# Kernel optimization log

Measured on AMD Instinct MI355X. Metric: run time of the kernel, lower is better.

## Reference

```python
import jax, jax.numpy as jnp
import numpy as np

EPS = 1e-14
RHO = 8.0


def _normalize(x):
    return x / jnp.linalg.norm(x, axis=-1, keepdims=True)


def setup_inputs() -> dict:
    key = jax.random.key(0)
    ks = jax.random.split(key, 12)
    B, D = 4096, 1024
    f = lambda k: _normalize(jax.random.normal(k, (B, D), dtype=jnp.float32))
    pos = lambda k: jax.random.uniform(k, (B, 1), dtype=jnp.float32, minval=0.1, maxval=1.0)
    return {
        "im_feat": f(ks[0]),
        "tt_feat": f(ks[1]),
        "rim_feat": f(ks[2]),
        "rtt_feat": f(ks[3]),
        "remote_u_im": pos(ks[4]),
        "remote_u_tt": pos(ks[5]),
        "loss1_im": pos(ks[6]),
        "loss1_tt": pos(ks[7]),
        "u_im": pos(ks[8]),
        "u_tt": pos(ks[9]),
        "logit_scale": 10.0 * jnp.ones((1,), dtype=jnp.float32),
        "offset": 0,
    }


def _pairwise_loss(rim, rtt, im, tt, logit_scale, offset):
    # features1 = remote, features2 = local (as in forward(): pairwise_loss(remote_features, features, ...))
    sim_image = rim @ tt.T                                  # [B1, B2]
    sim_text = rtt @ im.T                                   # [B1, B2]
    diag_sim = jnp.sum(rim * rtt, axis=-1, keepdims=True)   # [B1, 1]
    exp_im = jnp.exp((sim_image - diag_sim) * logit_scale)
    exp_tt = jnp.exp((sim_text - diag_sim) * logit_scale)
    B1, B2 = sim_image.shape
    # mask zeros the shifted diagonal: equivalent to subtracting the diagonal entry from the row sum
    cols = (jnp.arange(B1) + offset)[:, None]               # [B1, 1]
    rw_sum = B2 - 1 if B1 <= B2 else B2 * (B1 - 1) / B1
    loss_im = (jnp.sum(exp_im, axis=-1, keepdims=True)
               - jnp.take_along_axis(exp_im, cols, axis=1)) / rw_sum
    loss_tt = (jnp.sum(exp_tt, axis=-1, keepdims=True)
               - jnp.take_along_axis(exp_tt, cols, axis=1)) / rw_sum
    return loss_im, loss_tt


def reference(im_feat, tt_feat, rim_feat, rtt_feat, remote_u_im, remote_u_tt,
              loss1_im, loss1_tt, u_im, u_tt, logit_scale, offset):
    loss2_im, loss2_tt = _pairwise_loss(rim_feat, rtt_feat, im_feat, tt_feat, logit_scale, offset)
    pg1 = loss1_im / (u_im + EPS) + loss1_tt / (u_tt + EPS)
    pg2 = loss2_im / (remote_u_im + EPS) + loss2_tt / (remote_u_tt + EPS)
    loss = (jnp.mean(pg1) + jnp.mean(pg2)) / 2
    # multiply_tau branch
    ls = logit_scale[0]
    loss = loss / jax.lax.stop_gradient(ls)
    loss = loss + RHO / ls
    loss = loss + jnp.mean(jnp.log(u_im) + jnp.log(u_tt)) / 2 / ls
    return loss
```

## Files before the change

kernel.cpp:

```cpp
#include <hip/hip_runtime.h>
#include <hip/hip_bf16.h>

#define EPSF 1e-14f
#define RHOF 8.0f

typedef __attribute__((ext_vector_type(4))) float f32x4;
typedef __attribute__((ext_vector_type(8))) int   i32x8;
typedef __attribute__((ext_vector_type(2))) unsigned long long u64x2;

#define AS_GLOBAL __attribute__((address_space(1)))
#define AS_LDS    __attribute__((address_space(3)))


__global__ __launch_bounds__(256) void prep_fp8(
    const float* __restrict__ im,  const float* __restrict__ tt,
    const float* __restrict__ rim, const float* __restrict__ rtt,
    unsigned char* __restrict__ bIm,  unsigned char* __restrict__ bTt,
    unsigned char* __restrict__ bRim, unsigned char* __restrict__ bRtt,
    float* __restrict__ S_im, float* __restrict__ S_tt,
    float* __restrict__ diag, float* __restrict__ red,
    int D, int spm )
{
    __shared__ unsigned char L[8 * 1024];
    const int b = blockIdx.x;
    const int tid = threadIdx.x;
    const int nConv = 4 * spm;
    if (b < nConv) {
        int mIdx = b / spm;
        int slab = b - mIdx * spm;
        const float* src = (mIdx == 0) ? rim : (mIdx == 1) ? tt
                          : (mIdx == 2) ? rtt : im;
        unsigned char* dst = (mIdx == 0) ? bRim : (mIdx == 1) ? bTt
                            : (mIdx == 2) ? bRtt : bIm;
        const float* srow = src + (size_t)slab * 8 * D;
        const int n4 = (8 * D) >> 2;
        for (int idx = tid; idx < n4; idx += 256) {
            float4 v = *(const float4*)(srow + idx * 4);
            int pk = __builtin_amdgcn_cvt_pk_fp8_f32(v.x, v.y, 0, false);
            pk     = __builtin_amdgcn_cvt_pk_fp8_f32(v.z, v.w, pk, true);
            *(int*)&L[idx * 4] = pk;
        }
        __syncthreads();
        const int kTiles = D >> 7;
        const int rb = (slab * 8) >> 7;
        const int r0loc = (slab * 8) & 127;
        for (int g = tid; g < (D >> 1); g += 256) {
            int kb  = g >> 6;
            int rem = g & 63;
            int rl  = rem >> 3;
            int p   = rem & 7;
            int r   = slab * 8 + rl;
            int c   = p ^ (r & 7);
            const unsigned char* lb = &L[rl * D + kb * 128 + c * 16];
            u64x2 o = *(const u64x2*)lb;
            char* outp = (char*)dst
                       + ((size_t)(rb * kTiles + kb) * 1024
                          + (size_t)(r0loc + rl) * 8 + p) * 16;
            *(u64x2*)outp = o;
        }
    } else {
        int db = b - nConv;
        if (db == 0 && tid < 8) red[tid] = 0.f;
        if (tid < 4) { S_im[db * 4 + tid] = 0.f; S_tt[db * 4 + tid] = 0.f; }
        int row  = db * 4 + (tid >> 6);
        int lane = tid & 63;
        const float* a = rim + (size_t)row * D;
        const float* c = rtt + (size_t)row * D;
        float s = 0.f;
        for (int k = lane * 4; k < D; k += 256) {
            float4 av = *(const float4*)(a + k);
            float4 cv = *(const float4*)(c + k);
            s += av.x * cv.x + av.y * cv.y + av.z * cv.z + av.w * cv.w;
        }
        #pragma unroll
        for (int m2 = 1; m2 < 64; m2 <<= 1) s += __shfl_xor(s, m2, 64);
        if (lane == 0) diag[row] = s;
    }
}

__global__ __launch_bounds__(256) void gemm_expsum(
    const unsigned char* __restrict__ A0, const unsigned char* __restrict__ B0,
    float* __restrict__ S0,
    const unsigned char* __restrict__ A1, const unsigned char* __restrict__ B1,
    float* __restrict__ S1,
    const float* __restrict__ logit_scale, const int* __restrict__ offset,
    int Bn, int D)
{
    const int z = blockIdx.z;
    const unsigned char* A = z ? A1 : A0;
    const unsigned char* B = z ? B1 : B0;
    float* S = z ? S1 : S0;

    __shared__ unsigned char As[2][16384];
    __shared__ unsigned char Bs[2][16384];

    const int tid  = threadIdx.x;
    const int wave = tid >> 6;
    const int lane = tid & 63;
    const int lo   = lane & 15;
    const int qd   = lane >> 4;
    const int m0   = (wave >> 1) * 64;
    const int n0   = (wave & 1) * 64;
    const int s0   = (2 * qd) ^ (lo & 7);
    const int offA = s0 * 16;
    const int offB = (s0 ^ 1) * 16;

    const int kTiles = D >> 7;
    const unsigned char* Atile = A + (size_t)blockIdx.y * kTiles * 16384;
    const unsigned char* Btile = B + (size_t)blockIdx.x * kTiles * 16384;

    auto stage = [&](int buf, const unsigned char* At, const unsigned char* Bt) {
        #pragma unroll
        for (int j = 0; j < 4; ++j) {
            int goff = (j * 256 + tid) * 16;
            int loff = j * 4096 + wave * 1024;
            __builtin_amdgcn_global_load_lds(
                (const AS_GLOBAL unsigned int*)(At + goff),
                (AS_LDS unsigned int*)&As[buf][loff], 16, 0, 0);
            __builtin_amdgcn_global_load_lds(
                (const AS_GLOBAL unsigned int*)(Bt + goff),
                (AS_LDS unsigned int*)&Bs[buf][loff], 16, 0, 0);
        }
    };

    f32x4 acc[4][4];
    #pragma unroll
    for (int i = 0; i < 4; ++i)
        #pragma unroll
        for (int j = 0; j < 4; ++j)
            acc[i][j] = (f32x4){0.f, 0.f, 0.f, 0.f};

    stage(0, Atile, Btile);
    __syncthreads();

    for (int kb = 0; kb < kTiles; ++kb) {
        const int cur = kb & 1;
        if (kb + 1 < kTiles)
            stage(1 - cur, Atile + 16384, Btile + 16384);

        i32x8 bq[4];
        #pragma unroll
        for (int t = 0; t < 4; ++t) {
            int rn = (n0 + 16 * t + lo) * 128;
            union { int4 h[2]; i32x8 v; } u;
            u.h[0] = *(const int4*)&Bs[cur][rn + offA];
            u.h[1] = *(const int4*)&Bs[cur][rn + offB];
            bq[t] = u.v;
        }
        #pragma unroll
        for (int ti = 0; ti < 4; ++ti) {
            int ra = (m0 + 16 * ti + lo) * 128;
            union { int4 h[2]; i32x8 v; } u;
            u.h[0] = *(const int4*)&As[cur][ra + offA];
            u.h[1] = *(const int4*)&As[cur][ra + offB];
            i32x8 af = u.v;
            #pragma unroll
            for (int tj = 0; tj < 4; ++tj)
                acc[ti][tj] = __builtin_amdgcn_mfma_scale_f32_16x16x128_f8f6f4(
                    af, bq[tj], acc[ti][tj],
                    0, 0,
                    0, 127,
                    0, 127);
        }
        __syncthreads();

        Atile += 16384;
        Btile += 16384;
    }

    const float ls = logit_scale[0];
    const int offs = offset[0];
    const int rowBase = blockIdx.y * 128;
    const int colBase = blockIdx.x * 128;
    #pragma unroll
    for (int ti = 0; ti < 4; ++ti) {
        #pragma unroll
        for (int r = 0; r < 4; ++r) {
            int gi = rowBase + m0 + 16 * ti + 4 * qd + r;
            float rs = 0.f;
            #pragma unroll
            for (int tj = 0; tj < 4; ++tj) {
                int gj = colBase + n0 + 16 * tj + lo;
                float e = __expf(ls * acc[ti][tj][r]);
                if (gj == gi + offs) e = 0.f;
                rs += e;
            }
            #pragma unroll
            for (int m = 1; m < 16; m <<= 1) rs += __shfl_xor(rs, m, 64);
            if (lo == 0) atomicAdd(&S[gi], rs);
        }
    }
}

__global__ __launch_bounds__(256) void final_kernel(
    const float* __restrict__ S_im, const float* __restrict__ S_tt,
    const float* __restrict__ diag,
    const float* __restrict__ ru_im, const float* __restrict__ ru_tt,
    const float* __restrict__ l1_im, const float* __restrict__ l1_tt,
    const float* __restrict__ u_im,  const float* __restrict__ u_tt,
    const float* __restrict__ logit_scale, float* __restrict__ red,
    float* __restrict__ out, int Bn)
{
    const float ls = logit_scale[0];
    const float inv_rw = 1.0f / (float)(Bn - 1);
    const int gid = blockIdx.x * 256 + threadIdx.x;
    float pg = 0.f, lg = 0.f;
    for (int i = gid; i < Bn; i += 8 * 256) {
        float p1 = l1_im[i] / (u_im[i] + EPSF) + l1_tt[i] / (u_tt[i] + EPSF);
        float dd = expf(-ls * diag[i]);
        float p2 = dd * S_im[i] * inv_rw / (ru_im[i] + EPSF)
                 + dd * S_tt[i] * inv_rw / (ru_tt[i] + EPSF);
        pg += p1 + p2;
        lg += logf(u_im[i]) + logf(u_tt[i]);
    }
    __shared__ float sp[256], sl[256];
    sp[threadIdx.x] = pg; sl[threadIdx.x] = lg;
    __syncthreads();
    for (int s = 128; s > 0; s >>= 1) {
        if (threadIdx.x < s) { sp[threadIdx.x] += sp[threadIdx.x + s];
                               sl[threadIdx.x] += sl[threadIdx.x + s]; }
        __syncthreads();
    }
    if (threadIdx.x == 0) {
        atomicAdd(&red[0], sp[0]);
        atomicAdd(&red[1], sl[0]);
        __threadfence();
        int t = atomicAdd((int*)&red[2], 1);
        if (t == gridDim.x - 1) {
            float pgSum = atomicAdd(&red[0], 0.f);
            float lgSum = atomicAdd(&red[1], 0.f);
            float loss = ((pgSum / (float)Bn) * 0.5f) / ls
                       + RHOF / ls
                       + (lgSum / (float)Bn) * 0.5f / ls;
            out[0] = loss;
        }
    }
}

extern "C" void kernel_launch(void* const* d_in, const int* in_sizes, int n_in,
                              void* d_out, int out_size, void* d_ws, size_t ws_size,
                              hipStream_t stream) {
    const float* im    = (const float*)d_in[0];
    const float* tt    = (const float*)d_in[1];
    const float* rim   = (const float*)d_in[2];
    const float* rtt   = (const float*)d_in[3];
    const float* ru_im = (const float*)d_in[4];
    const float* ru_tt = (const float*)d_in[5];
    const float* l1_im = (const float*)d_in[6];
    const float* l1_tt = (const float*)d_in[7];
    const float* u_im  = (const float*)d_in[8];
    const float* u_tt  = (const float*)d_in[9];
    const float* lsc   = (const float*)d_in[10];
    const int*   offs  = (const int*)d_in[11];

    const int Bn = in_sizes[4];
    const int D  = in_sizes[0] / Bn;
    const int spm = Bn / 8;

    char* base = (char*)d_ws;
    float* S_im = (float*)base;
    float* S_tt = S_im + Bn;
    float* diag = S_tt + Bn;
    float* red  = diag + Bn;
    const size_t headBytes = (((size_t)(3 * Bn + 8) * sizeof(float)) + 255) & ~(size_t)255;
    const size_t matBytes  = (size_t)Bn * D;
    unsigned char* buf0 = (unsigned char*)(base + headBytes);
    unsigned char* bRim = buf0;
    unsigned char* bTt  = buf0 + matBytes;
    unsigned char* bRtt = buf0 + 2 * matBytes;
    unsigned char* bIm  = buf0 + 3 * matBytes;

    prep_fp8<<<4 * spm + Bn / 4, 256, 0, stream>>>(
        im, tt, rim, rtt, bIm, bTt, bRim, bRtt, S_im, S_tt, diag, red, D, spm);

    dim3 ggrid(Bn / 128, Bn / 128, 2);
    gemm_expsum<<<ggrid, 256, 0, stream>>>(bRim, bTt, S_im, bRtt, bIm, S_tt,
                                           lsc, offs, Bn, D);

    final_kernel<<<8, 256, 0, stream>>>(S_im, S_tt, diag, ru_im, ru_tt,
                                        l1_im, l1_tt, u_im, u_tt, lsc,
                                        red, (float*)d_out, Bn);
}
```

Baseline: 184.4 us.

## Enlarge GEMM tile to 256x256 with 8 waves, grid swizzle and MFMA priority

The fused fp8 GEMM+exp-sum kernel moves from 128x128 tiles with 4 waves to 256x256 tiles with 8 waves. Each wave now computes a 128x64 sub-tile, which raises operand reuse from LDS and cuts global traffic per output. The change also adds an XCD-style workgroup swizzle for L2 locality and wraps the MFMA loop in s_setprio. In exchange, LDS use rises to 128KB per block, accumulator registers double, and the grid shrinks to 512 blocks, so occupancy and tail effects may suffer.

```diff
diff --git a/kernel.cpp b/kernel.cpp
--- a/kernel.cpp
+++ b/kernel.cpp
@@ -78,7 +78,7 @@
     }
 }
 
-__global__ __launch_bounds__(256) void gemm_expsum(
+__global__ __launch_bounds__(512, 2) void gemm_expsum(
     const unsigned char* __restrict__ A0, const unsigned char* __restrict__ B0,
     float* __restrict__ S0,
     const unsigned char* __restrict__ A1, const unsigned char* __restrict__ B1,
@@ -91,69 +91,81 @@
     const unsigned char* B = z ? B1 : B0;
     float* S = z ? S1 : S0;
 
-    __shared__ unsigned char As[2][16384];
-    __shared__ unsigned char Bs[2][16384];
+    __shared__ unsigned char As[2][32768];
+    __shared__ unsigned char Bs[2][32768];
 
     const int tid  = threadIdx.x;
     const int wave = tid >> 6;
     const int lane = tid & 63;
     const int lo   = lane & 15;
     const int qd   = lane >> 4;
-    const int m0   = (wave >> 1) * 64;
-    const int n0   = (wave & 1) * 64;
-    const int s0   = (2 * qd) ^ (lo & 7);
-    const int offA = s0 * 16;
-    const int offB = (s0 ^ 1) * 16;
+    const int wm   = wave >> 2;
+    const int wn   = wave & 3;
+    const int offA = ((2 * qd) ^ (lo & 7)) * 16;
+
+    const int nx  = gridDim.x;
+    const int nwg = nx * gridDim.y;
+    int wg = blockIdx.y * nx + blockIdx.x;
+    int swz = ((nwg & 7) == 0) ? ((wg & 7) * (nwg >> 3) + (wg >> 3)) : wg;
+    const int by = swz / nx;
+    const int bx = swz - by * nx;
 
     const int kTiles = D >> 7;
-    const unsigned char* Atile = A + (size_t)blockIdx.y * kTiles * 16384;
-    const unsigned char* Btile = B + (size_t)blockIdx.x * kTiles * 16384;
-
-    auto stage = [&](int buf, const unsigned char* At, const unsigned char* Bt) {
-        #pragma unroll
-        for (int j = 0; j < 4; ++j) {
-            int goff = (j * 256 + tid) * 16;
-            int loff = j * 4096 + wave * 1024;
-            __builtin_amdgcn_global_load_lds(
-                (const AS_GLOBAL unsigned int*)(At + goff),
-                (AS_LDS unsigned int*)&As[buf][loff], 16, 0, 0);
-            __builtin_amdgcn_global_load_lds(
-                (const AS_GLOBAL unsigned int*)(Bt + goff),
-                (AS_LDS unsigned int*)&Bs[buf][loff], 16, 0, 0);
+    const unsigned char* Atile = A + (size_t)(2 * by) * kTiles * 16384;
+    const unsigned char* Btile = B + (size_t)(2 * bx) * kTiles * 16384;
+
+    auto stage = [&](int buf, int kb) {
+        #pragma unroll
+        for (int h = 0; h < 2; ++h) {
+            const size_t tbase = (size_t)(h * kTiles + kb) * 16384;
+            #pragma unroll
+            for (int i = 0; i < 2; ++i) {
+                const int u    = (i * 512 + tid) * 16;
+                const int loff = h * 16384 + i * 8192 + wave * 1024;
+                __builtin_amdgcn_global_load_lds(
+                    (const AS_GLOBAL unsigned int*)(Atile + tbase + u),
+                    (AS_LDS unsigned int*)&As[buf][loff], 16, 0, 0);
+                __builtin_amdgcn_global_load_lds(
+                    (const AS_GLOBAL unsigned int*)(Btile + tbase + u),
+                    (AS_LDS unsigned int*)&Bs[buf][loff], 16, 0, 0);
+            }
         }
     };
 
-    f32x4 acc[4][4];
+    f32x4 acc[8][4];
     #pragma unroll
-    for (int i = 0; i < 4; ++i)
+    for (int i = 0; i < 8; ++i)
         #pragma unroll
         for (int j = 0; j < 4; ++j)
             acc[i][j] = (f32x4){0.f, 0.f, 0.f, 0.f};
 
-    stage(0, Atile, Btile);
+    const int aOff0 = wm * 16384 + lo * 128 + offA;
+    const int bOff0 = (wn >> 1) * 16384 + ((wn & 1) * 64 + lo) * 128 + offA;
+
+    stage(0, 0);
     __syncthreads();
 
     for (int kb = 0; kb < kTiles; ++kb) {
         const int cur = kb & 1;
         if (kb + 1 < kTiles)
-            stage(1 - cur, Atile + 16384, Btile + 16384);
-
+            stage(1 - cur, kb + 1);
         i32x8 bq[4];
         #pragma unroll
-        for (int t = 0; t < 4; ++t) {
-            int rn = (n0 + 16 * t + lo) * 128;
+        for (int tj = 0; tj < 4; ++tj) {
+            const int ba = bOff0 + tj * 2048;
             union { int4 h[2]; i32x8 v; } u;
-            u.h[0] = *(const int4*)&Bs[cur][rn + offA];
-            u.h[1] = *(const int4*)&Bs[cur][rn + offB];
-            bq[t] = u.v;
-        }
-        #pragma unroll
-        for (int ti = 0; ti < 4; ++ti) {
-            int ra = (m0 + 16 * ti + lo) * 128;
+            u.h[0] = *(const int4*)&Bs[cur][ba];
+            u.h[1] = *(const int4*)&Bs[cur][ba ^ 16];
+            bq[tj] = u.v;
+        }
+        #pragma unroll
+        for (int ti = 0; ti < 8; ++ti) {
+            const int aa = aOff0 + ti * 2048;
             union { int4 h[2]; i32x8 v; } u;
-            u.h[0] = *(const int4*)&As[cur][ra + offA];
-            u.h[1] = *(const int4*)&As[cur][ra + offB];
+            u.h[0] = *(const int4*)&As[cur][aa];
+            u.h[1] = *(const int4*)&As[cur][aa ^ 16];
             i32x8 af = u.v;
+            __builtin_amdgcn_s_setprio(1);
             #pragma unroll
             for (int tj = 0; tj < 4; ++tj)
                 acc[ti][tj] = __builtin_amdgcn_mfma_scale_f32_16x16x128_f8f6f4(
@@ -161,26 +173,24 @@
                     0, 0,
                     0, 127,
                     0, 127);
+            __builtin_amdgcn_s_setprio(0);
         }
         __syncthreads();
-
-        Atile += 16384;
-        Btile += 16384;
     }
 
     const float ls = logit_scale[0];
     const int offs = offset[0];
-    const int rowBase = blockIdx.y * 128;
-    const int colBase = blockIdx.x * 128;
+    const int rowBase = by * 256 + wm * 128;
+    const int colBase = bx * 256 + wn * 64;
     #pragma unroll
-    for (int ti = 0; ti < 4; ++ti) {
+    for (int ti = 0; ti < 8; ++ti) {
         #pragma unroll
         for (int r = 0; r < 4; ++r) {
-            int gi = rowBase + m0 + 16 * ti + 4 * qd + r;
+            int gi = rowBase + 16 * ti + 4 * qd + r;
             float rs = 0.f;
             #pragma unroll
             for (int tj = 0; tj < 4; ++tj) {
-                int gj = colBase + n0 + 16 * tj + lo;
+                int gj = colBase + 16 * tj + lo;
                 float e = __expf(ls * acc[ti][tj][r]);
                 if (gj == gi + offs) e = 0.f;
                 rs += e;
@@ -273,8 +283,8 @@
     prep_fp8<<<4 * spm + Bn / 4, 256, 0, stream>>>(
         im, tt, rim, rtt, bIm, bTt, bRim, bRtt, S_im, S_tt, diag, red, D, spm);
 
-    dim3 ggrid(Bn / 128, Bn / 128, 2);
-    gemm_expsum<<<ggrid, 256, 0, stream>>>(bRim, bTt, S_im, bRtt, bIm, S_tt,
+    dim3 ggrid(Bn / 256, Bn / 256, 2);
+    gemm_expsum<<<ggrid, 512, 0, stream>>>(bRim, bTt, S_im, bRtt, bIm, S_tt,
                                            lsc, offs, Bn, D);
 
     final_kernel<<<8, 256, 0, stream>>>(S_im, S_tt, diag, ru_im, ru_tt,
```

Result: no change. 181.9 us (-1.4%).
